# Performance work log

Hardware: AMD Instinct MI355X
Metric: run time of the kernel (lower is better)

Reference implementation:

```python
import jax, jax.numpy as jnp
import numpy as np

HIDDEN = 5120
NUM_HEADS = 32
Q_LORA = 1536
KV_LORA = 512
NOPE = 128
ROPE = 64
V_DIM = 128
QK = NOPE + ROPE  # 192
T = 2048
ROPE_BASE = 10000.0
EPS = 1e-6


def setup_inputs() -> dict:
    key = jax.random.key(0)
    ks = jax.random.split(key, 8)
    s = 0.02
    return {
        "positions": jnp.arange(T, dtype=jnp.int64 if jax.config.jax_enable_x64 else jnp.int32),
        "hidden_states": jax.random.normal(ks[0], (T, HIDDEN), dtype=jnp.float32),
        "w_q_a": jax.random.normal(ks[1], (HIDDEN, Q_LORA), dtype=jnp.float32) * s,
        "q_a_norm": jnp.ones((Q_LORA,), dtype=jnp.float32),
        "w_q_b": jax.random.normal(ks[2], (Q_LORA, NUM_HEADS * QK), dtype=jnp.float32) * s,
        "w_kv_a": jax.random.normal(ks[3], (HIDDEN, KV_LORA + ROPE), dtype=jnp.float32) * s,
        "kv_a_norm": jnp.ones((KV_LORA,), dtype=jnp.float32),
        "w_kv_b": jax.random.normal(ks[4], (KV_LORA, NUM_HEADS * (NOPE + V_DIM)), dtype=jnp.float32) * s,
        "w_o": jax.random.normal(ks[5], (NUM_HEADS * V_DIM, HIDDEN), dtype=jnp.float32) * s,
    }


def _rmsnorm(x, w):
    var = jnp.mean(x * x, axis=-1, keepdims=True)
    return x * jax.lax.rsqrt(var + EPS) * w


def _rope_interleaved(x, positions):
    # x: [T, H, ROPE]; interleaved (GPT-J style) rotation, pairs (x[2i], x[2i+1])
    half = ROPE // 2
    inv_freq = 1.0 / (ROPE_BASE ** (jnp.arange(half, dtype=jnp.float32) * 2.0 / ROPE))
    angles = positions.astype(jnp.float32)[:, None] * inv_freq[None, :]  # [T, half]
    cos = jnp.cos(angles)[:, None, :]  # [T, 1, half]
    sin = jnp.sin(angles)[:, None, :]
    x1 = x[..., 0::2]
    x2 = x[..., 1::2]
    r1 = x1 * cos - x2 * sin
    r2 = x1 * sin + x2 * cos
    return jnp.stack([r1, r2], axis=-1).reshape(x.shape)


def reference(positions, hidden_states, w_q_a, q_a_norm, w_q_b, w_kv_a, kv_a_norm, w_kv_b, w_o):
    # Q path: down-proj -> RMSNorm -> up-proj -> split(nope, rope)
    q_c = _rmsnorm(hidden_states @ w_q_a, q_a_norm)
    q = (q_c @ w_q_b).reshape(T, NUM_HEADS, QK)
    q_nope, q_rope = q[:, :, :NOPE], q[:, :, NOPE:]

    # KV path: joint down-proj -> split(compressed, k_rope) -> RMSNorm -> up-proj
    kv_a = hidden_states @ w_kv_a
    compressed = _rmsnorm(kv_a[:, :KV_LORA], kv_a_norm)
    k_rope_raw = kv_a[:, KV_LORA:].reshape(T, 1, ROPE)
    kv = (compressed @ w_kv_b).reshape(T, NUM_HEADS, NOPE + V_DIM)
    k_nope, v = kv[:, :, :NOPE], kv[:, :, NOPE:]

    # RoPE on rope slices only (interleaved style since rope_interleave=True)
    q_rope = _rope_interleaved(q_rope, positions)
    k_rope = _rope_interleaved(k_rope_raw, positions)
    k_rope = jnp.broadcast_to(k_rope, (T, NUM_HEADS, ROPE))

    q_full = jnp.concatenate([q_nope, q_rope], axis=-1)  # [T, H, QK]
    k_full = jnp.concatenate([k_nope, k_rope], axis=-1)  # [T, H, QK]

    # Causal attention (RadixAttention prefill), scaling = qk_head_dim**-0.5.
    # v is zero-padded to QK in the source and sliced back after; using v
    # directly is mathematically identical.
    scale = QK ** (-0.5)
    scores = jnp.einsum("thd,shd->hts", q_full, k_full) * scale  # [H, T, T]
    causal = positions[:, None] >= positions[None, :]
    scores = jnp.where(causal[None, :, :], scores, jnp.float32(-1e30))
    probs = jax.nn.softmax(scores, axis=-1)
    attn = jnp.einsum("hts,shd->thd", probs, v)  # [T, H, V_DIM]

    out = attn.reshape(T, NUM_HEADS * V_DIM) @ w_o  # [T, HIDDEN]
    return out
```

## Files before the change

kernel.cpp:

```cpp
#include <hip/hip_runtime.h>

typedef unsigned short u16;
typedef unsigned int   u32;
typedef __bf16 bf16x8 __attribute__((ext_vector_type(8)));
typedef float  f32x4  __attribute__((ext_vector_type(4)));
typedef u16    u16x4  __attribute__((ext_vector_type(4)));
typedef u16    u16x8  __attribute__((ext_vector_type(8)));

__device__ __forceinline__ u16 f2bf(float f) {
  u32 u = __float_as_uint(f);
  u32 r = u + 0x7fffu + ((u >> 16) & 1u);
  return (u16)(r >> 16);
}

__device__ __forceinline__ void gl16(const void* g, void* l) {
  __builtin_amdgcn_global_load_lds((__attribute__((address_space(1))) void*)(g),
                                   (__attribute__((address_space(3))) void*)(l),
                                   16, 0, 0);
}

#define WAITVM4  asm volatile("s_waitcnt vmcnt(4)" ::: "memory")
#define WAITVM0  asm volatile("s_waitcnt vmcnt(0)" ::: "memory")
#define WAITLG0  asm volatile("s_waitcnt lgkmcnt(0)" ::: "memory")
#define BAR()    asm volatile("s_barrier" ::: "memory")
#define SCHEDB() __builtin_amdgcn_sched_barrier(0)

__device__ __forceinline__ void tr_tile(const float* __restrict__ W, u16* __restrict__ Wt,
                                        int K, int N, int NT, int idx, float (*tile)[65]) {
  const int tid = threadIdx.x;
  const int nt = idx % NT, kt = idx / NT;
  const int n0 = nt * 64, k0 = kt * 32;
  {
    const int r = tid >> 3, c8 = (tid & 7) << 3;
    const float* src = W + (size_t)(k0 + r) * N + n0 + c8;
    float4 a = *(const float4*)src;
    float4 b = *(const float4*)(src + 4);
    tile[r][c8 + 0] = a.x; tile[r][c8 + 1] = a.y; tile[r][c8 + 2] = a.z; tile[r][c8 + 3] = a.w;
    tile[r][c8 + 4] = b.x; tile[r][c8 + 5] = b.y; tile[r][c8 + 6] = b.z; tile[r][c8 + 7] = b.w;
  }
  __syncthreads();
  const int n = tid >> 2, kg = (tid & 3) << 3;
  u16x8 o;
  #pragma unroll
  for (int j = 0; j < 8; ++j) o[j] = f2bf(tile[kg + j][n]);
  *(u16x8*)(Wt + (size_t)(n0 + n) * K + k0 + kg) = o;
}

__global__ __launch_bounds__(256) void prep_w(const float* __restrict__ hidden, u16* __restrict__ hs_bf,
                                              const float* __restrict__ wqa,
                                              const float* __restrict__ wkva, u16* __restrict__ wab_t,
                                              const float* __restrict__ wqb,  u16* __restrict__ wqb_t,
                                              const float* __restrict__ wkvb, u16* __restrict__ wkvb_t,
                                              const float* __restrict__ wo,   u16* __restrict__ wo_t) {
  __shared__ float tile[32][65];
  const int b = blockIdx.x, tid = threadIdx.x;
  if (b < 640) {
    const float4* xin = (const float4*)hidden;
    #pragma unroll
    for (int j = 0; j < 8; ++j) {
      int u = b * 2048 + j * 256 + tid;
      float4 a = xin[u * 2], c = xin[u * 2 + 1];
      u16x8 o;
      o[0] = f2bf(a.x); o[1] = f2bf(a.y); o[2] = f2bf(a.z); o[3] = f2bf(a.w);
      o[4] = f2bf(c.x); o[5] = f2bf(c.y); o[6] = f2bf(c.z); o[7] = f2bf(c.w);
      *(u16x8*)(hs_bf + (size_t)u * 8) = o;
    }
  } else if (b < 4480) {
    tr_tile(wqa, wab_t, 5120, 1536, 24, b - 640, tile);
  } else if (b < 5920) {
    tr_tile(wkva, wab_t + (size_t)1536 * 5120, 5120, 576, 9, b - 4480, tile);
  } else if (b < 10528) {
    tr_tile(wqb, wqb_t, 1536, 6144, 96, b - 5920, tile);
  } else if (b < 12576) {
    tr_tile(wkvb, wkvb_t, 512, 8192, 128, b - 10528, tile);
  } else if (b < 22816) {
    tr_tile(wo, wo_t, 4096, 5120, 80, b - 12576, tile);
  } else {
    size_t off = (size_t)(b - 22816) * 4096 + tid * 16;
    u16x8 z = {};
    *(u16x8*)((char*)wab_t + (size_t)2112 * 5120 * 2 + off) = z;
  }
}

template<int EPI>
__device__ __forceinline__ void gemm8_body(char* lds,
                                           const u16* __restrict__ A,
                                           const u16* __restrict__ Bt,
                                           int N, int K, int wg, int nwg, int nbx,
                                           int nkt, int kt0,
                                           const int* __restrict__ pos,
                                           u16* __restrict__ q_all,
                                           u16* __restrict__ k_all,
                                           u16* __restrict__ v_big,
                                           float* __restrict__ Cf) {
  const int tid = threadIdx.x;
  const int lane = tid & 63, wid = tid >> 6;
  const int wr = wid >> 2, wc = wid & 3;
  const int lr = lane & 15, lg = lane >> 4;

  const int swz = ((nwg & 7) == 0) ? ((wg & 7) * (nwg >> 3) + (wg >> 3)) : wg;
  const int bx = swz % nbx, by = swz / nbx;
  const int m0 = by << 8, n0 = bx << 8;

  const size_t rs = (size_t)K << 1;
  const char* Ab = (const char*)A;
  const char* Bb = (const char*)Bt;

  const int sofs = tid << 4;
  const int srow = sofs >> 7;
  const int scol = ((((sofs >> 4) & 7) ^ (srow & 7)) << 4);

  const int axor = lr & 7;
  const int sx0 = (lg ^ axor) << 4;
  const int sx1 = ((4 | lg) ^ axor) << 4;
  const int bcolbase = (wc & 1) << 13;

  f32x4 acc[8][4] = {};

#define ASL(p,h) ((((p) << 1) | (h)) << 14)
#define BSL(p,h) (65536 + ((((p) << 1) | (h)) << 14))
#define STAGE_HALF(gb, grow0, kt, slot)                                              \
  { const char* _s = (gb) + (size_t)(grow0) * rs + ((size_t)((kt) + kt0) << 7) + scol; \
    gl16(_s, lds + (slot) + sofs);                                                   \
    gl16(_s + (rs << 6), lds + (slot) + sofs + 8192); }

  STAGE_HALF(Ab, m0 + srow,       0, ASL(0,0));
  STAGE_HALF(Ab, m0 + 128 + srow, 0, ASL(0,1));
  STAGE_HALF(Bb, n0 + srow,       0, BSL(0,0));
  STAGE_HALF(Bb, n0 + 128 + srow, 0, BSL(0,1));
  if (nkt > 1) {
    STAGE_HALF(Bb, n0 + srow,       1, BSL(1,0));
    STAGE_HALF(Bb, n0 + 128 + srow, 1, BSL(1,1));
    WAITVM4;
  } else {
    WAITVM0;
  }
  BAR();

  for (int b = 0; b < nkt; ++b) {
    const int p = b & 1;
    const int abase = ASL(p, wr);
    const int bbase = BSL(p, (wc >> 1)) + bcolbase;
    bf16x8 aR[4][2], bR[4][2];

    #pragma unroll
    for (int m = 0; m < 4; ++m) {
      aR[m][0] = *(const bf16x8*)(lds + abase + (m * 16 + lr) * 128 + sx0);
      aR[m][1] = *(const bf16x8*)(lds + abase + (m * 16 + lr) * 128 + sx1);
    }
    #pragma unroll
    for (int n = 0; n < 2; ++n) {
      bR[n][0] = *(const bf16x8*)(lds + bbase + (n * 16 + lr) * 128 + sx0);
      bR[n][1] = *(const bf16x8*)(lds + bbase + (n * 16 + lr) * 128 + sx1);
    }
    if (b + 1 < nkt) { STAGE_HALF(Ab, m0 + srow, b + 1, ASL((b + 1) & 1, 0)); }
    BAR(); WAITLG0; SCHEDB();
    __builtin_amdgcn_s_setprio(1);
    #pragma unroll
    for (int kf = 0; kf < 2; ++kf)
      #pragma unroll
      for (int m = 0; m < 4; ++m)
        #pragma unroll
        for (int n = 0; n < 2; ++n)
          acc[m][n] = __builtin_amdgcn_mfma_f32_16x16x32_bf16(aR[m][kf], bR[n][kf], acc[m][n], 0, 0, 0);
    __builtin_amdgcn_s_setprio(0); SCHEDB();
    BAR();

    #pragma unroll
    for (int n = 2; n < 4; ++n) {
      bR[n][0] = *(const bf16x8*)(lds + bbase + (n * 16 + lr) * 128 + sx0);
      bR[n][1] = *(const bf16x8*)(lds + bbase + (n * 16 + lr) * 128 + sx1);
    }
    if (b + 1 < nkt) { STAGE_HALF(Ab, m0 + 128 + srow, b + 1, ASL((b + 1) & 1, 1)); }
    BAR(); WAITLG0; SCHEDB();
    __builtin_amdgcn_s_setprio(1);
    #pragma unroll
    for (int kf = 0; kf < 2; ++kf)
      #pragma unroll
      for (int m = 0; m < 4; ++m)
        #pragma unroll
        for (int n = 2; n < 4; ++n)
          acc[m][n] = __builtin_amdgcn_mfma_f32_16x16x32_bf16(aR[m][kf], bR[n][kf], acc[m][n], 0, 0, 0);
    __builtin_amdgcn_s_setprio(0); SCHEDB();
    BAR();

    #pragma unroll
    for (int m = 0; m < 4; ++m) {
      aR[m][0] = *(const bf16x8*)(lds + abase + ((m + 4) * 16 + lr) * 128 + sx0);
      aR[m][1] = *(const bf16x8*)(lds + abase + ((m + 4) * 16 + lr) * 128 + sx1);
    }
    if (b + 2 < nkt) { STAGE_HALF(Bb, n0 + srow, b + 2, BSL(p, 0)); }
    BAR(); WAITLG0; SCHEDB();
    __builtin_amdgcn_s_setprio(1);
    #pragma unroll
    for (int kf = 0; kf < 2; ++kf)
      #pragma unroll
      for (int m = 0; m < 4; ++m)
        #pragma unroll
        for (int n = 0; n < 2; ++n)
          acc[m + 4][n] = __builtin_amdgcn_mfma_f32_16x16x32_bf16(aR[m][kf], bR[n][kf], acc[m + 4][n], 0, 0, 0);
    __builtin_amdgcn_s_setprio(0); SCHEDB();
    BAR();

    if (b + 2 < nkt) { STAGE_HALF(Bb, n0 + 128 + srow, b + 2, BSL(p, 1)); }
    BAR(); SCHEDB();
    __builtin_amdgcn_s_setprio(1);
    #pragma unroll
    for (int kf = 0; kf < 2; ++kf)
      #pragma unroll
      for (int m = 0; m < 4; ++m)
        #pragma unroll
        for (int n = 2; n < 4; ++n)
          acc[m + 4][n] = __builtin_amdgcn_mfma_f32_16x16x32_bf16(aR[m][kf], bR[n][kf], acc[m + 4][n], 0, 0, 0);
    __builtin_amdgcn_s_setprio(0); SCHEDB();
    if (b + 2 < nkt) { WAITVM4; } else { WAITVM0; }
    BAR();
  }

  if (EPI == 0) {
    #pragma unroll
    for (int m = 0; m < 8; ++m) {
      const int row0 = m0 + wr * 128 + m * 16 + lg * 4;
      #pragma unroll
      for (int n = 0; n < 4; ++n) {
        const int col = n0 + wc * 64 + n * 16 + lr;
        #pragma unroll
        for (int r = 0; r < 4; ++r)
          Cf[(size_t)(row0 + r) * N + col] = acc[m][n][r];
      }
    }
  } else if (EPI == 1) {
    int hh[4], dd[4]; float inv[4]; bool rope[4];
    #pragma unroll
    for (int n = 0; n < 4; ++n) {
      int col = n0 + wc * 64 + n * 16 + lr;
      hh[n] = col / 192;
      dd[n] = col - hh[n] * 192;
      rope[n] = (dd[n] >= 128);
      int i = (dd[n] - 128) >> 1;
      inv[n] = rope[n] ? exp2f(-(float)i * 0.41524101186092f) : 0.f;
    }
    const bool odd = (lr & 1);
    #pragma unroll
    for (int m = 0; m < 8; ++m) {
      const int row0 = m0 + wr * 128 + m * 16 + lg * 4;
      #pragma unroll
      for (int r = 0; r < 4; ++r) {
        const int row = row0 + r;
        const float pv = (float)pos[row];
        #pragma unroll
        for (int n = 0; n < 4; ++n) {
          float v = acc[m][n][r];
          float o = __shfl_xor(v, 1, 64);
          if (rope[n]) {
            float s, c;
            __sincosf(pv * inv[n], &s, &c);
            v = odd ? (o * s + v * c) : (v * c - o * s);
          }
          q_all[((size_t)hh[n] * 2048 + row) * 192 + dd[n]] = f2bf(v);
        }
      }
    }
  } else {
    #pragma unroll
    for (int m = 0; m < 8; ++m) {
      const int row0 = m0 + wr * 128 + m * 16 + lg * 4;
      #pragma unroll
      for (int r = 0; r < 4; ++r) {
        const int row = row0 + r;
        #pragma unroll
        for (int n = 0; n < 4; ++n) {
          const int col = n0 + wc * 64 + n * 16 + lr;
          const int h = col >> 8, dd = col & 255;
          u16 bv = f2bf(acc[m][n][r]);
          if (dd < 128) k_all[((size_t)h * 2048 + row) * 200 + dd] = bv;
          else          v_big[(size_t)row * 4096 + h * 128 + (dd - 128)] = bv;
        }
      }
    }
  }
#undef ASL
#undef BSL
#undef STAGE_HALF
}

#define SLAB2 ((size_t)2048 * 2304)
__global__ __launch_bounds__(512, 2) void gemm_a8(const u16* __restrict__ A,
                                                  const u16* __restrict__ Bt,
                                                  float* __restrict__ C) {
  __shared__ char lds[131072];
  const int z = blockIdx.x / 72;
  const int wg = blockIdx.x - z * 72;
  const int nkt = (z == 2) ? 26 : 27;
  const int kt0 = z * 27;
  gemm8_body<0>(lds, A, Bt, 2304, 5120, wg, 72, 9, nkt, kt0,
                nullptr, nullptr, nullptr, nullptr, C + (size_t)z * SLAB2);
}

__global__ __launch_bounds__(512, 2) void gemm_fused_b(const u16* __restrict__ A1,
                                                       const u16* __restrict__ B1,
                                                       const u16* __restrict__ A2,
                                                       const u16* __restrict__ B2,
                                                       const int* __restrict__ pos,
                                                       u16* __restrict__ q_all,
                                                       u16* __restrict__ k_all,
                                                       u16* __restrict__ v_big) {
  __shared__ char lds[131072];
  if (blockIdx.x < 192)
    gemm8_body<1>(lds, A1, B1, 6144, 1536, blockIdx.x, 192, 24, 24, 0, pos, q_all, nullptr, nullptr, nullptr);
  else
    gemm8_body<2>(lds, A2, B2, 8192, 512, blockIdx.x - 192, 256, 32, 8, 0, pos, nullptr, k_all, v_big, nullptr);
}

__global__ __launch_bounds__(512, 2) void gemm_out_k(const u16* __restrict__ A,
                                                     const u16* __restrict__ Bt,
                                                     float* __restrict__ C) {
  __shared__ char lds[131072];
  gemm8_body<0>(lds, A, Bt, 5120, 4096, blockIdx.x, 160, 20, 64, 0,
                nullptr, nullptr, nullptr, nullptr, C);
}

__global__ __launch_bounds__(256) void norm_q_kernel(const float* __restrict__ x,
                                                     const float* __restrict__ w,
                                                     u16* __restrict__ y) {
  const int row = blockIdx.x, tid = threadIdx.x;
  const float* xr = x + (size_t)row * 2304;
  float v[6]; float ss = 0.f;
  #pragma unroll
  for (int i = 0; i < 6; ++i) {
    size_t o = tid + i * 256;
    v[i] = xr[o] + xr[o + SLAB2] + xr[o + 2 * SLAB2];
    ss += v[i] * v[i];
  }
  __shared__ float sm[4];
  #pragma unroll
  for (int o = 32; o > 0; o >>= 1) ss += __shfl_down(ss, o, 64);
  if ((tid & 63) == 0) sm[tid >> 6] = ss;
  __syncthreads();
  float tot = sm[0] + sm[1] + sm[2] + sm[3];
  float rs = rsqrtf(tot * (1.f / 1536.f) + 1e-6f);
  #pragma unroll
  for (int i = 0; i < 6; ++i)
    y[(size_t)row * 1536 + tid + i * 256] = f2bf(v[i] * rs * w[tid + i * 256]);
}

__global__ __launch_bounds__(256) void norm_kv_kernel(const float* __restrict__ kva,
                                                      const float* __restrict__ w,
                                                      const int* __restrict__ pos,
                                                      u16* __restrict__ comp,
                                                      u16* __restrict__ krope) {
  const int row = blockIdx.x, tid = threadIdx.x;
  const float* xr = kva + (size_t)row * 2304 + 1536;
  float v0 = xr[tid] + xr[tid + SLAB2] + xr[tid + 2 * SLAB2];
  size_t o1 = tid + 256;
  float v1 = xr[o1] + xr[o1 + SLAB2] + xr[o1 + 2 * SLAB2];
  float ss = v0 * v0 + v1 * v1;
  __shared__ float sm[4];
  #pragma unroll
  for (int o = 32; o > 0; o >>= 1) ss += __shfl_down(ss, o, 64);
  if ((tid & 63) == 0) sm[tid >> 6] = ss;
  __syncthreads();
  float tot = sm[0] + sm[1] + sm[2] + sm[3];
  float rs = rsqrtf(tot * (1.f / 512.f) + 1e-6f);
  comp[(size_t)row * 512 + tid]       = f2bf(v0 * rs * w[tid]);
  comp[(size_t)row * 512 + tid + 256] = f2bf(v1 * rs * w[tid + 256]);
  if (tid < 32) {
    float p = (float)pos[row];
    float inv = powf(10000.0f, -(float)(2 * tid) * (1.0f / 64.0f));
    float ang = p * inv;
    float c = cosf(ang), s = sinf(ang);
    size_t e1 = 512 + 2 * tid, e2 = e1 + 1;
    float x1 = xr[e1] + xr[e1 + SLAB2] + xr[e1 + 2 * SLAB2];
    float x2 = xr[e2] + xr[e2 + SLAB2] + xr[e2 + 2 * SLAB2];
    krope[(size_t)row * 64 + 2 * tid]     = f2bf(x1 * c - x2 * s);
    krope[(size_t)row * 64 + 2 * tid + 1] = f2bf(x1 * s + x2 * c);
  }
}

__global__ __launch_bounds__(256) void krope_bcast(const u16* __restrict__ krope,
                                                   u16* __restrict__ k_all) {
  const int s = blockIdx.x, tid = threadIdx.x;
  const int h = tid >> 3, j8 = (tid & 7) << 3;
  *(u16x8*)&k_all[((size_t)h * 2048 + s) * 200 + 128 + j8] =
      *(const u16x8*)&krope[(size_t)s * 64 + j8];
}

__global__ __launch_bounds__(256) void v_transpose(const u16* __restrict__ v_big,
                                                   u16* __restrict__ v_t) {
  const int h = blockIdx.x & 31, st = blockIdx.x >> 5, tid = threadIdx.x;
  const int s0 = st * 64;
  __shared__ u16 vs[64][128];
  for (int idx = tid; idx < 4096; idx += 256) {
    int s = idx >> 6, d2 = idx & 63;
    *(u32*)&vs[s][d2 * 2] = *(const u32*)&v_big[(size_t)(s0 + s) * 4096 + h * 128 + d2 * 2];
  }
  __syncthreads();
  const int d = tid >> 1, sh = (tid & 1) * 32;
  u16 tmp[32];
  #pragma unroll
  for (int i = 0; i < 32; ++i) tmp[i] = vs[sh + i][d];
  #pragma unroll
  for (int b = 0; b < 4; ++b) {
    u16x8 o;
    #pragma unroll
    for (int j = 0; j < 8; ++j) o[j] = tmp[b * 8 + j];
    *(u16x8*)(v_t + ((size_t)h * 128 + d) * 2048 + s0 + sh + b * 8) = o;
  }
}

#define SCL2 0.10412706f
#define THR2 11.5f
__global__ __launch_bounds__(512, 2) void attn_fwd(const u16* __restrict__ q_all,
                                                   const u16* __restrict__ k_all,
                                                   const u16* __restrict__ v_t,
                                                   u16* __restrict__ attnb) {
  __shared__ __align__(16) char lds[106496];
  const int tid = threadIdx.x;
  const int lane = tid & 63, wid = tid >> 6;
  const int lr = lane & 15, lg = lane >> 4;
  const int h = blockIdx.x & 31, bq = blockIdx.x >> 5;

  const char* kh = (const char*)(k_all + (size_t)h * 2048 * 200);
  const char* vh = (const char*)(v_t + (size_t)h * 128 * 2048);
  char* Pw = lds + 88064 + wid * 2304;

  const int nCalls = (wid < 3) ? 6 : 5;
  const char* gp[6]; int cofs[6]; int isK[6];
  #pragma unroll
  for (int ii = 0; ii < 6; ++ii) {
    int i = wid + (ii << 3);
    if (i < 43) {
      int c = (i << 6) + lane;
      cofs[ii] = c << 4;
      if (c < 1600) { gp[ii] = kh + ((size_t)c << 4); isK[ii] = 1; }
      else {
        int cv = c - 1600;
        int row = cv / 9, sub = cv - row * 9;
        gp[ii] = vh + ((size_t)row << 12) + ((sub < 8) ? (sub << 4) : 0);
        isK[ii] = 0;
      }
    } else { gp[ii] = kh; cofs[ii] = 0; isK[ii] = 1; }
  }

#define STAGE(s0_, bOff_)                                                       \
  { int _sk = (s0_) * 400, _sv = (s0_) * 2;                                     \
    _Pragma("unroll")                                                           \
    for (int ii = 0; ii < 6; ++ii)                                              \
      if (ii < nCalls)                                                          \
        gl16(gp[ii] + (isK[ii] ? _sk : _sv), lds + (bOff_) + cofs[ii]); }

#define WAITSTAGE                                                               \
  { if (wid < 3) { asm volatile("s_waitcnt vmcnt(6)" ::: "memory"); }           \
    else        { asm volatile("s_waitcnt vmcnt(5)" ::: "memory"); } }

  const int kRd = lr * 400 + lg * 16;
  const int vRd = lr * 144 + lg * 16;
  const int pRd = lr * 144 + lg * 16;
  const int pWr = lr * 144 + lg * 8;

  #pragma unroll
  for (int half = 0; half < 2; ++half) {
    const int qt = half ? (15 - bq) : bq;
    const int qb0 = qt << 7;
    const int nt = 2 * qt + 2;
    const int qlane = qb0 + wid * 16 + lr;
    const int qwmin = qb0 + wid * 16;

    bf16x8 qf[6];
    const u16* qptr = q_all + ((size_t)h * 2048 + qlane) * 192 + lg * 8;
    #pragma unroll
    for (int kf = 0; kf < 6; ++kf) qf[kf] = *(const bf16x8*)(qptr + kf * 32);

    f32x4 O[8] = {};
    float m = -1e30f, l = 0.f;

    STAGE(0, 0);
    for (int st = 0; st < nt; ++st) {
      const int s0 = st << 6;
      const int bOff = (st & 1) * 44032;
      if (st + 1 < nt) {
        STAGE((st + 1) << 6, ((st + 1) & 1) * 44032);
        WAITSTAGE;
      } else {
        WAITVM0;
      }
      BAR();

      const bool active = (s0 <= qwmin + 15);
      if (active) {
        const char* Kb = lds + bOff;
        const char* Vb = lds + bOff + 25600;

        f32x4 S[4];
        #pragma unroll
        for (int sb = 0; sb < 4; ++sb) {
          f32x4 a = {};
          #pragma unroll
          for (int kf = 0; kf < 6; ++kf) {
            bf16x8 kfr = *(const bf16x8*)(Kb + kRd + sb * 6400 + kf * 64);
            a = __builtin_amdgcn_mfma_f32_16x16x32_bf16(kfr, qf[kf], a, 0, 0, 0);
          }
          S[sb] = a;
        }

        if (s0 + 63 > qwmin) {
          const int kb0 = s0 + lg * 4;
          #pragma unroll
          for (int sb = 0; sb < 4; ++sb)
            #pragma unroll
            for (int r = 0; r < 4; ++r) {
              int k = kb0 + sb * 16 + r;
              S[sb][r] = (k > qlane) ? -1e30f : S[sb][r] * SCL2;
            }
        } else {
          #pragma unroll
          for (int sb = 0; sb < 4; ++sb)
            #pragma unroll
            for (int r = 0; r < 4; ++r) S[sb][r] *= SCL2;
        }

        float mx = S[0][0];
        #pragma unroll
        for (int sb = 0; sb < 4; ++sb)
          #pragma unroll
          for (int r = 0; r < 4; ++r) mx = fmaxf(mx, S[sb][r]);
        mx = fmaxf(mx, __shfl_xor(mx, 16, 64));
        mx = fmaxf(mx, __shfl_xor(mx, 32, 64));

        const bool skip = __all(mx <= m + THR2);
        float alpha = 1.f;
        if (!skip) { float mn = fmaxf(m, mx); alpha = exp2f(m - mn); m = mn; }

        float ps = 0.f;
        #pragma unroll
        for (int sb = 0; sb < 4; ++sb)
          #pragma unroll
          for (int r = 0; r < 4; ++r) {
            float pv = exp2f(S[sb][r] - m);
            S[sb][r] = pv;
            ps += pv;
          }
        ps += __shfl_xor(ps, 16, 64);
        ps += __shfl_xor(ps, 32, 64);
        l = l * alpha + ps;

        if (!skip) {
          float aO[4];
          #pragma unroll
          for (int r = 0; r < 4; ++r) aO[r] = __shfl(alpha, lg * 4 + r, 64);
          #pragma unroll
          for (int nb = 0; nb < 8; ++nb)
            #pragma unroll
            for (int r = 0; r < 4; ++r) O[nb][r] *= aO[r];
        }

        #pragma unroll
        for (int sb = 0; sb < 4; ++sb) {
          u32 p01, p23;
          asm("v_cvt_pk_bf16_f32 %0, %1, %2" : "=v"(p01) : "v"(S[sb][0]), "v"(S[sb][1]));
          asm("v_cvt_pk_bf16_f32 %0, %1, %2" : "=v"(p23) : "v"(S[sb][2]), "v"(S[sb][3]));
          *(uint2*)(Pw + pWr + sb * 32) = make_uint2(p01, p23);
        }

        #pragma unroll
        for (int k2 = 0; k2 < 2; ++k2) {
          bf16x8 pa = *(const bf16x8*)(Pw + pRd + k2 * 64);
          #pragma unroll
          for (int nb = 0; nb < 8; ++nb) {
            bf16x8 vf = *(const bf16x8*)(Vb + vRd + nb * 2304 + k2 * 64);
            O[nb] = __builtin_amdgcn_mfma_f32_16x16x32_bf16(pa, vf, O[nb], 0, 0, 0);
          }
        }
      }
      BAR();
    }

    float rv[4];
    #pragma unroll
    for (int r = 0; r < 4; ++r) rv[r] = 1.f / __shfl(l, lg * 4 + r, 64);
    #pragma unroll
    for (int nb = 0; nb < 8; ++nb) {
      const int col = h * 128 + nb * 16 + lr;
      #pragma unroll
      for (int r = 0; r < 4; ++r)
        attnb[(size_t)(qb0 + wid * 16 + lg * 4 + r) * 4096 + col] = f2bf(O[nb][r] * rv[r]);
    }
  }
#undef STAGE
#undef WAITSTAGE
}

extern "C" void kernel_launch(void* const* d_in, const int* in_sizes, int n_in,
                              void* d_out, int out_size, void* d_ws, size_t ws_size,
                              hipStream_t stream) {
  const int*   positions = (const int*)d_in[0];
  const float* hidden    = (const float*)d_in[1];
  const float* w_q_a     = (const float*)d_in[2];
  const float* q_a_norm  = (const float*)d_in[3];
  const float* w_q_b     = (const float*)d_in[4];
  const float* w_kv_a    = (const float*)d_in[5];
  const float* kv_a_norm = (const float*)d_in[6];
  const float* w_kv_b    = (const float*)d_in[7];
  const float* w_o       = (const float*)d_in[8];
  float* out = (float*)d_out;
  char*  ws  = (char*)d_ws;

  u16* hs_bf  = (u16*)(ws + 0);
  u16* attnb  = (u16*)(ws + 0);
  u16* wab_t  = (u16*)(ws + 20971520);
  u16* q_c_n  = (u16*)(ws + 20971520);
  u16* comp   = (u16*)(ws + 27262976);
  u16* krope  = (u16*)(ws + 29360128);
  u16* wqb_t  = (u16*)(ws + 44564480);
  u16* wkvb_t = (u16*)(ws + 63438848);
  u16* wo_t   = (u16*)(ws + 71827456);
  float* slabs = (float*)(ws + 113770496);
  u16* q_all  = (u16*)(ws + 113770496);
  u16* k_all  = (u16*)(ws + 138936320);
  u16* v_big  = (u16*)(ws + 170393600);
  u16* v_t    = (u16*)(ws + 187170816);

  prep_w<<<23296, 256, 0, stream>>>(hidden, hs_bf, w_q_a, w_kv_a, wab_t,
                                    w_q_b, wqb_t, w_kv_b, wkvb_t, w_o, wo_t);

  gemm_a8<<<216, 512, 0, stream>>>(hs_bf, wab_t, slabs);

  norm_q_kernel<<<2048, 256, 0, stream>>>(slabs, q_a_norm, q_c_n);
  norm_kv_kernel<<<2048, 256, 0, stream>>>(slabs, kv_a_norm, positions, comp, krope);
  krope_bcast<<<2048, 256, 0, stream>>>(krope, k_all);

  gemm_fused_b<<<448, 512, 0, stream>>>(q_c_n, wqb_t, comp, wkvb_t, positions,
                                        q_all, k_all, v_big);

  v_transpose<<<1024, 256, 0, stream>>>(v_big, v_t);

  attn_fwd<<<256, 512, 0, stream>>>(q_all, k_all, v_t, attnb);

  gemm_out_k<<<160, 512, 0, stream>>>(attnb, wo_t, out);
}
```

Baseline: 399.3 us.

## Overlap weight conversion with first GEMM, fuse norm kernels, add MFMA priority

The bf16 transpose of w_q_b, w_kv_b and w_o moves out of the prep kernel and into extra blocks of the first GEMM launch, so it can run alongside the down-projection GEMM. Each extra block handles 33 tiles in two 256-thread halves. The q-norm, kv-norm/rope and k-rope broadcast kernels are merged into one per-row kernel, which removes two launches and the krope round trip through memory. The attention kernel also raises wave priority around its MFMA sections. The cost is that the transpose blocks compete with the GEMM for CUs and LDS.

```diff
diff --git a/kernel.cpp b/kernel.cpp
--- a/kernel.cpp
+++ b/kernel.cpp
@@ -46,12 +46,9 @@
   *(u16x8*)(Wt + (size_t)(n0 + n) * K + k0 + kg) = o;
 }
 
-__global__ __launch_bounds__(256) void prep_w(const float* __restrict__ hidden, u16* __restrict__ hs_bf,
+__global__ __launch_bounds__(256) void prep_a(const float* __restrict__ hidden, u16* __restrict__ hs_bf,
                                               const float* __restrict__ wqa,
-                                              const float* __restrict__ wkva, u16* __restrict__ wab_t,
-                                              const float* __restrict__ wqb,  u16* __restrict__ wqb_t,
-                                              const float* __restrict__ wkvb, u16* __restrict__ wkvb_t,
-                                              const float* __restrict__ wo,   u16* __restrict__ wo_t) {
+                                              const float* __restrict__ wkva, u16* __restrict__ wab_t) {
   __shared__ float tile[32][65];
   const int b = blockIdx.x, tid = threadIdx.x;
   if (b < 640) {
@@ -69,14 +66,8 @@
     tr_tile(wqa, wab_t, 5120, 1536, 24, b - 640, tile);
   } else if (b < 5920) {
     tr_tile(wkva, wab_t + (size_t)1536 * 5120, 5120, 576, 9, b - 4480, tile);
-  } else if (b < 10528) {
-    tr_tile(wqb, wqb_t, 1536, 6144, 96, b - 5920, tile);
-  } else if (b < 12576) {
-    tr_tile(wkvb, wkvb_t, 512, 8192, 128, b - 10528, tile);
-  } else if (b < 22816) {
-    tr_tile(wo, wo_t, 4096, 5120, 80, b - 12576, tile);
   } else {
-    size_t off = (size_t)(b - 22816) * 4096 + tid * 16;
+    size_t off = (size_t)(b - 5920) * 4096 + tid * 16;
     u16x8 z = {};
     *(u16x8*)((char*)wab_t + (size_t)2112 * 5120 * 2 + off) = z;
   }
@@ -285,16 +276,56 @@
 }
 
 #define SLAB2 ((size_t)2048 * 2304)
-__global__ __launch_bounds__(512, 2) void gemm_a8(const u16* __restrict__ A,
-                                                  const u16* __restrict__ Bt,
-                                                  float* __restrict__ C) {
+__global__ __launch_bounds__(512, 2) void gemm_a8p(const u16* __restrict__ A,
+                                                   const u16* __restrict__ Bt,
+                                                   float* __restrict__ C,
+                                                   const float* __restrict__ wqb,  u16* __restrict__ wqb_t,
+                                                   const float* __restrict__ wkvb, u16* __restrict__ wkvb_t,
+                                                   const float* __restrict__ wo,   u16* __restrict__ wo_t) {
   __shared__ char lds[131072];
-  const int z = blockIdx.x / 72;
-  const int wg = blockIdx.x - z * 72;
-  const int nkt = (z == 2) ? 26 : 27;
-  const int kt0 = z * 27;
-  gemm8_body<0>(lds, A, Bt, 2304, 5120, wg, 72, 9, nkt, kt0,
-                nullptr, nullptr, nullptr, nullptr, C + (size_t)z * SLAB2);
+  const int b = blockIdx.x;
+  if (b < 216) {
+    const int z = b / 72;
+    const int wg = b - z * 72;
+    const int nkt = (z == 2) ? 26 : 27;
+    gemm8_body<0>(lds, A, Bt, 2304, 5120, wg, 72, 9, nkt, z * 27,
+                  nullptr, nullptr, nullptr, nullptr, C + (size_t)z * SLAB2);
+  } else {
+    float (*tile)[32][65] = (float (*)[32][65])lds;
+    const int pb = b - 216;
+    const int sub = threadIdx.x >> 8, t = threadIdx.x & 255;
+    for (int i = 0; i < 17; ++i) {
+      const int li = 2 * i + sub;
+      const bool ok = (li < 33);
+      const float* W = nullptr; u16* Wt = nullptr; int K = 0, N = 0, NT = 1, idx = 0;
+      if (ok) {
+        int gt = pb * 33 + li;
+        if (gt < 4608)      { W = wqb;  Wt = wqb_t;  K = 1536; N = 6144; NT = 96;  idx = gt; }
+        else if (gt < 6656) { W = wkvb; Wt = wkvb_t; K = 512;  N = 8192; NT = 128; idx = gt - 4608; }
+        else                { W = wo;   Wt = wo_t;   K = 4096; N = 5120; NT = 80;  idx = gt - 6656; }
+        const int nt = idx % NT, kt = idx / NT;
+        const int n0 = nt * 64, k0 = kt * 32;
+        const int r = t >> 3, c8 = (t & 7) << 3;
+        const float* src = W + (size_t)(k0 + r) * N + n0 + c8;
+        float4 a = *(const float4*)src;
+        float4 bb = *(const float4*)(src + 4);
+        float* tr = tile[sub][r];
+        tr[c8 + 0] = a.x;  tr[c8 + 1] = a.y;  tr[c8 + 2] = a.z;  tr[c8 + 3] = a.w;
+        tr[c8 + 4] = bb.x; tr[c8 + 5] = bb.y; tr[c8 + 6] = bb.z; tr[c8 + 7] = bb.w;
+      }
+      __syncthreads();
+      if (ok) {
+        const int nt = idx % NT, kt = idx / NT;
+        const int n0 = nt * 64, k0 = kt * 32;
+        const int n = t >> 2, kg = (t & 3) << 3;
+        u16x8 o;
+        #pragma unroll
+        for (int j = 0; j < 8; ++j) o[j] = f2bf(tile[sub][kg + j][n]);
+        *(u16x8*)(Wt + (size_t)(n0 + n) * K + k0 + kg) = o;
+      }
+      __syncthreads();
+    }
+  }
 }
 
 __global__ __launch_bounds__(512, 2) void gemm_fused_b(const u16* __restrict__ A1,
@@ -320,11 +351,18 @@
                 nullptr, nullptr, nullptr, nullptr, C);
 }
 
-__global__ __launch_bounds__(256) void norm_q_kernel(const float* __restrict__ x,
-                                                     const float* __restrict__ w,
-                                                     u16* __restrict__ y) {
+__global__ __launch_bounds__(256) void norm_all(const float* __restrict__ slabs,
+                                                const float* __restrict__ wq,
+                                                const float* __restrict__ wkv,
+                                                const int* __restrict__ pos,
+                                                u16* __restrict__ q_c_n,
+                                                u16* __restrict__ comp,
+                                                u16* __restrict__ k_all) {
   const int row = blockIdx.x, tid = threadIdx.x;
-  const float* xr = x + (size_t)row * 2304;
+  const float* xr = slabs + (size_t)row * 2304;
+  __shared__ float sm[4];
+  __shared__ u16 krv[64];
+
   float v[6]; float ss = 0.f;
   #pragma unroll
   for (int i = 0; i < 6; ++i) {
@@ -332,57 +370,42 @@
     v[i] = xr[o] + xr[o + SLAB2] + xr[o + 2 * SLAB2];
     ss += v[i] * v[i];
   }
-  __shared__ float sm[4];
   #pragma unroll
   for (int o = 32; o > 0; o >>= 1) ss += __shfl_down(ss, o, 64);
   if ((tid & 63) == 0) sm[tid >> 6] = ss;
   __syncthreads();
-  float tot = sm[0] + sm[1] + sm[2] + sm[3];
-  float rs = rsqrtf(tot * (1.f / 1536.f) + 1e-6f);
+  float rsq = rsqrtf((sm[0] + sm[1] + sm[2] + sm[3]) * (1.f / 1536.f) + 1e-6f);
   #pragma unroll
   for (int i = 0; i < 6; ++i)
-    y[(size_t)row * 1536 + tid + i * 256] = f2bf(v[i] * rs * w[tid + i * 256]);
-}
-
-__global__ __launch_bounds__(256) void norm_kv_kernel(const float* __restrict__ kva,
-                                                      const float* __restrict__ w,
-                                                      const int* __restrict__ pos,
-                                                      u16* __restrict__ comp,
-                                                      u16* __restrict__ krope) {
-  const int row = blockIdx.x, tid = threadIdx.x;
-  const float* xr = kva + (size_t)row * 2304 + 1536;
-  float v0 = xr[tid] + xr[tid + SLAB2] + xr[tid + 2 * SLAB2];
+    q_c_n[(size_t)row * 1536 + tid + i * 256] = f2bf(v[i] * rsq * wq[tid + i * 256]);
+
+  const float* xk = xr + 1536;
+  float v0 = xk[tid] + xk[tid + SLAB2] + xk[tid + 2 * SLAB2];
   size_t o1 = tid + 256;
-  float v1 = xr[o1] + xr[o1 + SLAB2] + xr[o1 + 2 * SLAB2];
-  float ss = v0 * v0 + v1 * v1;
-  __shared__ float sm[4];
-  #pragma unroll
-  for (int o = 32; o > 0; o >>= 1) ss += __shfl_down(ss, o, 64);
-  if ((tid & 63) == 0) sm[tid >> 6] = ss;
+  float v1 = xk[o1] + xk[o1 + SLAB2] + xk[o1 + 2 * SLAB2];
+  float ss2 = v0 * v0 + v1 * v1;
+  #pragma unroll
+  for (int o = 32; o > 0; o >>= 1) ss2 += __shfl_down(ss2, o, 64);
   __syncthreads();
-  float tot = sm[0] + sm[1] + sm[2] + sm[3];
-  float rs = rsqrtf(tot * (1.f / 512.f) + 1e-6f);
-  comp[(size_t)row * 512 + tid]       = f2bf(v0 * rs * w[tid]);
-  comp[(size_t)row * 512 + tid + 256] = f2bf(v1 * rs * w[tid + 256]);
+  if ((tid & 63) == 0) sm[tid >> 6] = ss2;
   if (tid < 32) {
     float p = (float)pos[row];
     float inv = powf(10000.0f, -(float)(2 * tid) * (1.0f / 64.0f));
     float ang = p * inv;
     float c = cosf(ang), s = sinf(ang);
     size_t e1 = 512 + 2 * tid, e2 = e1 + 1;
-    float x1 = xr[e1] + xr[e1 + SLAB2] + xr[e1 + 2 * SLAB2];
-    float x2 = xr[e2] + xr[e2 + SLAB2] + xr[e2 + 2 * SLAB2];
-    krope[(size_t)row * 64 + 2 * tid]     = f2bf(x1 * c - x2 * s);
-    krope[(size_t)row * 64 + 2 * tid + 1] = f2bf(x1 * s + x2 * c);
-  }
-}
-
-__global__ __launch_bounds__(256) void krope_bcast(const u16* __restrict__ krope,
-                                                   u16* __restrict__ k_all) {
-  const int s = blockIdx.x, tid = threadIdx.x;
+    float x1 = xk[e1] + xk[e1 + SLAB2] + xk[e1 + 2 * SLAB2];
+    float x2 = xk[e2] + xk[e2 + SLAB2] + xk[e2 + 2 * SLAB2];
+    krv[2 * tid]     = f2bf(x1 * c - x2 * s);
+    krv[2 * tid + 1] = f2bf(x1 * s + x2 * c);
+  }
+  __syncthreads();
+  float rsk = rsqrtf((sm[0] + sm[1] + sm[2] + sm[3]) * (1.f / 512.f) + 1e-6f);
+  comp[(size_t)row * 512 + tid]       = f2bf(v0 * rsk * wkv[tid]);
+  comp[(size_t)row * 512 + tid + 256] = f2bf(v1 * rsk * wkv[tid + 256]);
+
   const int h = tid >> 3, j8 = (tid & 7) << 3;
-  *(u16x8*)&k_all[((size_t)h * 2048 + s) * 200 + 128 + j8] =
-      *(const u16x8*)&krope[(size_t)s * 64 + j8];
+  *(u16x8*)&k_all[((size_t)h * 2048 + row) * 200 + 128 + j8] = *(const u16x8*)&krv[j8];
 }
 
 __global__ __launch_bounds__(256) void v_transpose(const u16* __restrict__ v_big,
@@ -492,6 +515,7 @@
         const char* Vb = lds + bOff + 25600;
 
         f32x4 S[4];
+        __builtin_amdgcn_s_setprio(1);
         #pragma unroll
         for (int sb = 0; sb < 4; ++sb) {
           f32x4 a = {};
@@ -502,6 +526,7 @@
           }
           S[sb] = a;
         }
+        __builtin_amdgcn_s_setprio(0);
 
         if (s0 + 63 > qwmin) {
           const int kb0 = s0 + lg * 4;
@@ -562,6 +587,7 @@
           *(uint2*)(Pw + pWr + sb * 32) = make_uint2(p01, p23);
         }
 
+        __builtin_amdgcn_s_setprio(1);
         #pragma unroll
         for (int k2 = 0; k2 < 2; ++k2) {
           bf16x8 pa = *(const bf16x8*)(Pw + pRd + k2 * 64);
@@ -571,6 +597,7 @@
             O[nb] = __builtin_amdgcn_mfma_f32_16x16x32_bf16(pa, vf, O[nb], 0, 0, 0);
           }
         }
+        __builtin_amdgcn_s_setprio(0);
       }
       BAR();
     }
@@ -610,7 +637,6 @@
   u16* wab_t  = (u16*)(ws + 20971520);
   u16* q_c_n  = (u16*)(ws + 20971520);
   u16* comp   = (u16*)(ws + 27262976);
-  u16* krope  = (u16*)(ws + 29360128);
   u16* wqb_t  = (u16*)(ws + 44564480);
   u16* wkvb_t = (u16*)(ws + 63438848);
   u16* wo_t   = (u16*)(ws + 71827456);
@@ -620,14 +646,13 @@
   u16* v_big  = (u16*)(ws + 170393600);
   u16* v_t    = (u16*)(ws + 187170816);
 
-  prep_w<<<23296, 256, 0, stream>>>(hidden, hs_bf, w_q_a, w_kv_a, wab_t,
+  prep_a<<<6400, 256, 0, stream>>>(hidden, hs_bf, w_q_a, w_kv_a, wab_t);
+
+  gemm_a8p<<<728, 512, 0, stream>>>(hs_bf, wab_t, slabs,
                                     w_q_b, wqb_t, w_kv_b, wkvb_t, w_o, wo_t);
 
-  gemm_a8<<<216, 512, 0, stream>>>(hs_bf, wab_t, slabs);
-
-  norm_q_kernel<<<2048, 256, 0, stream>>>(slabs, q_a_norm, q_c_n);
-  norm_kv_kernel<<<2048, 256, 0, stream>>>(slabs, kv_a_norm, positions, comp, krope);
-  krope_bcast<<<2048, 256, 0, stream>>>(krope, k_all);
+  norm_all<<<2048, 256, 0, stream>>>(slabs, q_a_norm, kv_a_norm, positions,
+                                     q_c_n, comp, k_all);
 
   gemm_fused_b<<<448, 512, 0, stream>>>(q_c_n, wqb_t, comp, wkvb_t, positions,
                                         q_all, k_all, v_big);
```

After: 415.8 us. 1.04x slower.
